# Kernel tuning notes

Measured on AMD Instinct MI355X. Metric: run time of the kernel, lower is better.

## Reference

```python
import jax, jax.numpy as jnp
import numpy as np

B, T, D, H = 2, 4096, 768, 12
HD = D // H  # head_dim = 64


def setup_inputs() -> dict:
    key = jax.random.key(0)
    ks = jax.random.split(key, 6)
    s = 0.02
    return {
        "x": jax.random.normal(ks[0], (B, T, D), dtype=jnp.float32),
        "Wq": jax.random.normal(ks[1], (D, D), dtype=jnp.float32) * s,
        "Wk": jax.random.normal(ks[2], (D, D), dtype=jnp.float32) * s,
        "Wv": jax.random.normal(ks[3], (D, D), dtype=jnp.float32) * s,
        "Wo": jax.random.normal(ks[4], (D, D), dtype=jnp.float32) * s,
        "bo": jnp.zeros((D,), dtype=jnp.float32),
    }


def reference(x, Wq, Wk, Wv, Wo, bo):
    b, t, d = x.shape
    # QKV projections (no bias), reshape to [B, H, T, HD]
    def heads(w):
        return (x @ w.T).reshape(b, t, H, HD).transpose(0, 2, 1, 3)
    q, k, v = heads(Wq), heads(Wk), heads(Wv)
    scores = jnp.einsum("bhqd,bhkd->bhqk", q, k)  # [B,H,T,T]
    causal = jnp.tril(jnp.ones((t, t), dtype=bool))
    scores = jnp.where(causal, scores, -jnp.inf)
    attn = jax.nn.softmax(scores / jnp.sqrt(jnp.float32(HD)), axis=-1)
    ctx = jnp.einsum("bhqk,bhkd->bhqd", attn, v)  # [B,H,T,HD]
    ctx = ctx.transpose(0, 2, 1, 3).reshape(b, t, d)
    return ctx @ Wo.T + bo
```

## Files before the change

kernel.cpp:

```cpp
#include <hip/hip_runtime.h>
#include <hip/hip_bf16.h>
#include <cstdint>
#include <cstddef>

#define B_  2
#define T_  4096
#define D_  768
#define H_  12
#define HD_ 64
#define M_  (B_*T_)

#define SCL 0.18033688f

typedef __bf16 bf16x8 __attribute__((ext_vector_type(8)));
typedef float  f32x4  __attribute__((ext_vector_type(4)));
using bf16 = __hip_bfloat16;

__device__ inline float fexp2(float x) {
  float r; asm("v_exp_f32 %0, %1" : "=v"(r) : "v"(x)); return r;
}
__device__ inline uint32_t fu(float x) { union { float f; uint32_t u; } c; c.f = x; return c.u; }
__device__ inline uint32_t pktr(float a, float b) {
  return __builtin_amdgcn_perm(fu(b), fu(a), 0x07060302);
}
#define GLD16(g, l) __builtin_amdgcn_global_load_lds( \
    (const __attribute__((address_space(1))) uint32_t*)(const void*)(g), \
    (__attribute__((address_space(3))) uint32_t*)(void*)(l), 16, 0, 0)

__global__ void cvt_all(const float* __restrict__ x,
                        const float* __restrict__ w0, const float* __restrict__ w1,
                        const float* __restrict__ w2, const float* __restrict__ w3,
                        bf16* __restrict__ xd,
                        bf16* __restrict__ d0, bf16* __restrict__ d1,
                        bf16* __restrict__ d2, bf16* __restrict__ d3) {
  int blk = blockIdx.x;
  const float* s; bf16* d; int i;
  if (blk < 6144) {
    s = x; d = xd; i = blk * 256 + threadIdx.x;
  } else {
    int q = blk - 6144, which = q / 576, rb = q % 576;
    switch (which) {
      case 0: s = w0; d = d0; break;
      case 1: s = w1; d = d1; break;
      case 2: s = w2; d = d2; break;
      default: s = w3; d = d3; break;
    }
    i = rb * 256 + threadIdx.x;
  }
  float4 v = ((const float4*)s)[i];
  union { bf16 o[4]; uint2 u; } pk;
  pk.o[0] = __float2bfloat16(v.x); pk.o[1] = __float2bfloat16(v.y);
  pk.o[2] = __float2bfloat16(v.z); pk.o[3] = __float2bfloat16(v.w);
  *(uint2*)(d + 4 * (size_t)i) = pk.u;
}

__global__ __launch_bounds__(256) void gemm_qkv(const bf16* __restrict__ x,
                                                const bf16* __restrict__ W0,
                                                const bf16* __restrict__ W1,
                                                const bf16* __restrict__ W2,
                                                bf16* __restrict__ O0,
                                                bf16* __restrict__ O1,
                                                bf16* __restrict__ O2t) {
  __shared__ bf16 As[2][4096];
  __shared__ bf16 Bs[2][4096];
  const int flat = blockIdx.x;
  const int by = flat / 18;
  const int rr = flat % 18;
  const int z  = rr / 6;
  const int bx = rr % 6;
  const bf16* Wz = (z == 0) ? W0 : ((z == 1) ? W1 : W2);
  const char* Ap; const char* Bp; int a0, b0;
  if (z == 2) { Ap = (const char*)x;  a0 = by * 128; Bp = (const char*)Wz; b0 = bx * 128; }
  else        { Ap = (const char*)Wz; a0 = bx * 128; Bp = (const char*)x;  b0 = by * 128; }
  const int t = threadIdx.x;
  const int w = t >> 6, lane = t & 63;
  const int wa = (w >> 1) * 64, wb = (w & 1) * 64;
  const int mi = lane & 15, qd = lane >> 4;

  int aoff[2], boff[2];
  #pragma unroll
  for (int i = 0; i < 2; ++i) {
    int L = i * 256 + t;
    int row = L >> 2, sl = L & 3, c = sl ^ (row & 3);
    aoff[i] = (a0 + row) * 1536 + c * 16;
    boff[i] = (b0 + row) * 1536 + c * 16;
  }
  const int fsw = (qd ^ (mi & 3)) * 8;

  f32x4 acc[4][4] = {};

  #pragma unroll
  for (int i = 0; i < 2; ++i) {
    GLD16(Ap + aoff[i], &As[0][i * 2048 + w * 512]);
    GLD16(Bp + boff[i], &Bs[0][i * 2048 + w * 512]);
  }

  for (int kk = 0; kk < 24; ++kk) {
    __syncthreads();
    const int par = kk & 1;
    if (kk + 1 < 24) {
      const int np = par ^ 1, kb = (kk + 1) * 64;
      #pragma unroll
      for (int i = 0; i < 2; ++i) {
        GLD16(Ap + aoff[i] + kb, &As[np][i * 2048 + w * 512]);
        GLD16(Bp + boff[i] + kb, &Bs[np][i * 2048 + w * 512]);
      }
    }
    bf16x8 af[4], bfr[4];
    #pragma unroll
    for (int at = 0; at < 4; ++at)
      af[at] = *(const bf16x8*)&As[par][(wa + at * 16 + mi) * 32 + fsw];
    #pragma unroll
    for (int bt = 0; bt < 4; ++bt)
      bfr[bt] = *(const bf16x8*)&Bs[par][(wb + bt * 16 + mi) * 32 + fsw];
    #pragma unroll
    for (int at = 0; at < 4; ++at)
      #pragma unroll
      for (int bt = 0; bt < 4; ++bt)
        acc[at][bt] = __builtin_amdgcn_mfma_f32_16x16x32_bf16(af[at], bfr[bt], acc[at][bt], 0, 0, 0);
  }

  if (z == 2) {
    #pragma unroll
    for (int at = 0; at < 4; ++at)
      #pragma unroll
      for (int bt = 0; bt < 4; ++bt) {
        int gr = a0 + wa + at * 16 + qd * 4;
        int gc = b0 + wb + bt * 16 + mi;
        union { bf16 o[4]; uint2 u; } pk;
        #pragma unroll
        for (int r = 0; r < 4; ++r) pk.o[r] = __float2bfloat16(acc[at][bt][r]);
        int bb = gr >> 12, tt = gr & 4095;
        *(uint2*)(O2t + (size_t)bb * 768 * 4096 + (size_t)gc * 4096 + tt) = pk.u;
      }
  } else {
    const float scl = (z == 1) ? SCL : 1.0f;
    bf16* Ob = (z == 0) ? O0 : O1;
    #pragma unroll
    for (int at = 0; at < 4; ++at)
      #pragma unroll
      for (int bt = 0; bt < 4; ++bt) {
        int f0  = a0 + wa + at * 16 + qd * 4;
        int tkn = b0 + wb + bt * 16 + mi;
        union { bf16 o[4]; uint2 u; } pk;
        #pragma unroll
        for (int r = 0; r < 4; ++r) pk.o[r] = __float2bfloat16(acc[at][bt][r] * scl);
        *(uint2*)(Ob + (size_t)tkn * 768 + f0) = pk.u;
      }
  }
}

__global__ __launch_bounds__(256) void gemm_out(const bf16* __restrict__ ctx,
                                                const bf16* __restrict__ Wo,
                                                float* __restrict__ Cf,
                                                const float* __restrict__ bias) {
  __shared__ bf16 As[2][4096];
  __shared__ bf16 Bs[2][4096];
  const int flat = blockIdx.x;
  const int by = flat / 6, bx = flat % 6;
  const char* Ap = (const char*)Wo;  const int a0 = bx * 128;
  const char* Bp = (const char*)ctx; const int b0 = by * 128;
  const int t = threadIdx.x;
  const int w = t >> 6, lane = t & 63;
  const int wa = (w >> 1) * 64, wb = (w & 1) * 64;
  const int mi = lane & 15, qd = lane >> 4;

  int aoff[2], boff[2];
  #pragma unroll
  for (int i = 0; i < 2; ++i) {
    int L = i * 256 + t;
    int row = L >> 2, sl = L & 3, c = sl ^ (row & 3);
    aoff[i] = (a0 + row) * 1536 + c * 16;
    boff[i] = (b0 + row) * 1536 + c * 16;
  }
  const int fsw = (qd ^ (mi & 3)) * 8;

  f32x4 acc[4][4] = {};

  #pragma unroll
  for (int i = 0; i < 2; ++i) {
    GLD16(Ap + aoff[i], &As[0][i * 2048 + w * 512]);
    GLD16(Bp + boff[i], &Bs[0][i * 2048 + w * 512]);
  }

  for (int kk = 0; kk < 24; ++kk) {
    __syncthreads();
    const int par = kk & 1;
    if (kk + 1 < 24) {
      const int np = par ^ 1, kb = (kk + 1) * 64;
      #pragma unroll
      for (int i = 0; i < 2; ++i) {
        GLD16(Ap + aoff[i] + kb, &As[np][i * 2048 + w * 512]);
        GLD16(Bp + boff[i] + kb, &Bs[np][i * 2048 + w * 512]);
      }
    }
    bf16x8 af[4], bfr[4];
    #pragma unroll
    for (int at = 0; at < 4; ++at)
      af[at] = *(const bf16x8*)&As[par][(wa + at * 16 + mi) * 32 + fsw];
    #pragma unroll
    for (int bt = 0; bt < 4; ++bt)
      bfr[bt] = *(const bf16x8*)&Bs[par][(wb + bt * 16 + mi) * 32 + fsw];
    #pragma unroll
    for (int at = 0; at < 4; ++at)
      #pragma unroll
      for (int bt = 0; bt < 4; ++bt)
        acc[at][bt] = __builtin_amdgcn_mfma_f32_16x16x32_bf16(af[at], bfr[bt], acc[at][bt], 0, 0, 0);
  }

  #pragma unroll
  for (int at = 0; at < 4; ++at)
    #pragma unroll
    for (int bt = 0; bt < 4; ++bt) {
      int f0  = a0 + wa + at * 16 + qd * 4;
      int tkn = b0 + wb + bt * 16 + mi;
      float4 bv = *(const float4*)&bias[f0];
      float4 o;
      o.x = acc[at][bt][0] + bv.x; o.y = acc[at][bt][1] + bv.y;
      o.z = acc[at][bt][2] + bv.z; o.w = acc[at][bt][3] + bv.w;
      *(float4*)&Cf[(size_t)tkn * 768 + f0] = o;
    }
}

__global__ __launch_bounds__(256, 4) void flash_attn(const bf16* __restrict__ Q,
                                                     const bf16* __restrict__ K,
                                                     const bf16* __restrict__ Vt,
                                                     bf16* __restrict__ ctx) {
  __shared__ bf16 Ks[2][4096];
  __shared__ bf16 Vs[2][4096];
  __shared__ bf16 Pt[4][1024];
  const int t = threadIdx.x;
  const int w = t >> 6, lane = t & 63;
  const int mi = lane & 15, qd = lane >> 4;
  const int bh   = blockIdx.x % 24;
  const int qrev = blockIdx.x / 24;
  const int q0 = T_ - 64 - qrev * 64;
  const int b = bh / H_, h = bh % H_;
  const size_t bTD = (size_t)b * T_ * D_;
  const char* Kp = (const char*)(K  + bTD + (size_t)h * HD_);
  const char* Vp = (const char*)(Vt + (size_t)b * D_ * T_ + (size_t)h * HD_ * T_);
  const int qw = q0 + w * 16;

  int vkoff[2], vvoff[2];
  #pragma unroll
  for (int i = 0; i < 2; ++i) {
    int L = i * 256 + t;
    int rl = L >> 3, c = (L & 7) ^ (rl & 7);
    vkoff[i] = rl * 1536 + c * 16;
    vvoff[i] = rl * 8192 + c * 16;
  }

  int fidx[4][2];
  #pragma unroll
  for (int jt = 0; jt < 4; ++jt)
    #pragma unroll
    for (int kt = 0; kt < 2; ++kt)
      fidx[jt][kt] = (jt * 16 + mi) * 64 + (((kt * 4 + qd) ^ (mi & 7)) * 8);

  int pwoff[4], proff[2];
  #pragma unroll
  for (int jt = 0; jt < 4; ++jt)
    pwoff[jt] = mi * 64 + ((2 * jt + (qd >> 1)) ^ (mi & 7)) * 8 + (qd & 1) * 4;
  #pragma unroll
  for (int kt = 0; kt < 2; ++kt)
    proff[kt] = mi * 64 + ((4 * kt + qd) ^ (mi & 7)) * 8;

  bf16x8 qf[2];
  const bf16* Qp = Q + bTD + (size_t)h * HD_;
  #pragma unroll
  for (int kt = 0; kt < 2; ++kt)
    qf[kt] = *(const bf16x8*)(Qp + (size_t)(qw + mi) * D_ + kt * 32 + qd * 8);

  f32x4 oacc[4] = {};
  float lst = 0.f;
  const int ntiles = q0 / 64 + 1;

  #pragma unroll
  for (int i = 0; i < 2; ++i) {
    GLD16(Kp + vkoff[i], &Ks[0][i * 2048 + w * 512]);
    GLD16(Vp + vvoff[i], &Vs[0][i * 2048 + w * 512]);
  }

  for (int tt = 0; tt < ntiles; ++tt) {
    __syncthreads();
    const int par = tt & 1;
    if (tt + 1 < ntiles) {
      const size_t j1 = (size_t)(tt + 1) * 64;
      const int np = par ^ 1;
      #pragma unroll
      for (int i = 0; i < 2; ++i) {
        GLD16(Kp + vkoff[i] + j1 * 1536, &Ks[np][i * 2048 + w * 512]);
        GLD16(Vp + vvoff[i] + j1 * 2,    &Vs[np][i * 2048 + w * 512]);
      }
    }
    const int j0 = tt * 64;

    f32x4 sacc[4] = {};
    #pragma unroll
    for (int jt = 0; jt < 4; ++jt)
      #pragma unroll
      for (int kt = 0; kt < 2; ++kt) {
        bf16x8 kf = *(const bf16x8*)&Ks[par][fidx[jt][kt]];
        sacc[jt] = __builtin_amdgcn_mfma_f32_16x16x32_bf16(kf, qf[kt], sacc[jt], 0, 0, 0);
      }

    if (j0 + 63 > qw) {
      const int qg = qw + mi;
      #pragma unroll
      for (int jt = 0; jt < 4; ++jt)
        #pragma unroll
        for (int r = 0; r < 4; ++r) {
          int jg = j0 + jt * 16 + qd * 4 + r;
          if (jg > qg) sacc[jt][r] = -1e30f;
        }
    }

    #pragma unroll
    for (int jt = 0; jt < 4; ++jt) {
      float p0 = fexp2(sacc[jt][0]);
      float p1 = fexp2(sacc[jt][1]);
      float p2 = fexp2(sacc[jt][2]);
      float p3 = fexp2(sacc[jt][3]);
      lst += (p0 + p1) + (p2 + p3);
      union { uint32_t u[2]; uint64_t d; } pw;
      pw.u[0] = pktr(p0, p1);
      pw.u[1] = pktr(p2, p3);
      *(uint64_t*)&Pt[w][pwoff[jt]] = pw.d;
    }

    asm volatile("s_waitcnt lgkmcnt(0)" ::: "memory");

    #pragma unroll
    for (int ktp = 0; ktp < 2; ++ktp) {
      bf16x8 pfx = *(const bf16x8*)&Pt[w][proff[ktp]];
      #pragma unroll
      for (int dt = 0; dt < 4; ++dt) {
        bf16x8 vf = *(const bf16x8*)&Vs[par][fidx[dt][ktp]];
        oacc[dt] = __builtin_amdgcn_mfma_f32_16x16x32_bf16(vf, pfx, oacc[dt], 0, 0, 0);
      }
    }
  }

  float l = lst;
  l += __shfl_xor(l, 16);
  l += __shfl_xor(l, 32);
  float inv = __builtin_amdgcn_rcpf(l);
  const int qg = qw + mi;
  bf16* cp = ctx + bTD + (size_t)qg * D_ + h * HD_ + qd * 4;
  #pragma unroll
  for (int dt = 0; dt < 4; ++dt) {
    union { bf16 o[4]; uint2 u; } pko;
    #pragma unroll
    for (int r = 0; r < 4; ++r) pko.o[r] = __float2bfloat16(oacc[dt][r] * inv);
    *(uint2*)(cp + dt * 16) = pko.u;
  }
}

extern "C" void kernel_launch(void* const* d_in, const int* in_sizes, int n_in,
                              void* d_out, int out_size, void* d_ws, size_t ws_size,
                              hipStream_t stream) {
  const float* x  = (const float*)d_in[0];
  const float* Wq = (const float*)d_in[1];
  const float* Wk = (const float*)d_in[2];
  const float* Wv = (const float*)d_in[3];
  const float* Wo = (const float*)d_in[4];
  const float* bo = (const float*)d_in[5];
  float* out = (float*)d_out;

  char* ws = (char*)d_ws;
  const size_t SZ  = (size_t)M_ * D_ * 2;
  const size_t WSZ = (size_t)D_ * D_ * 2;
  bf16* xb   = (bf16*)(ws);
  bf16* Qb   = (bf16*)(ws + 1 * SZ);
  bf16* Kb   = (bf16*)(ws + 2 * SZ);
  bf16* Vtg  = (bf16*)(ws + 3 * SZ);
  bf16* ctxb = (bf16*)(ws + 4 * SZ);
  bf16* Wqb  = (bf16*)(ws + 5 * SZ);
  bf16* Wkb  = (bf16*)(ws + 5 * SZ + 1 * WSZ);
  bf16* Wvb  = (bf16*)(ws + 5 * SZ + 2 * WSZ);
  bf16* Wob  = (bf16*)(ws + 5 * SZ + 3 * WSZ);

  cvt_all<<<6144 + 4 * 576, 256, 0, stream>>>(x, Wq, Wk, Wv, Wo, xb, Wqb, Wkb, Wvb, Wob);

  gemm_qkv<<<1152, 256, 0, stream>>>(xb, Wqb, Wkb, Wvb, Qb, Kb, Vtg);

  flash_attn<<<(T_ / 64) * B_ * H_, 256, 0, stream>>>(Qb, Kb, Vtg, ctxb);

  gemm_out<<<384, 256, 0, stream>>>(ctxb, Wob, out, bo);
}
```

Before: 244.0 us.

## Keep attention probabilities in registers via permuted K rows; retile output GEMM

```diff
diff --git a/kernel.cpp b/kernel.cpp
--- a/kernel.cpp
+++ b/kernel.cpp
@@ -154,62 +154,61 @@
                                                 const bf16* __restrict__ Wo,
                                                 float* __restrict__ Cf,
                                                 const float* __restrict__ bias) {
-  __shared__ bf16 As[2][4096];
+  __shared__ bf16 As[2][2048];
   __shared__ bf16 Bs[2][4096];
   const int flat = blockIdx.x;
-  const int by = flat / 6, bx = flat % 6;
-  const char* Ap = (const char*)Wo;  const int a0 = bx * 128;
+  const int by = flat / 12, bx = flat % 12;
+  const char* Ap = (const char*)Wo;  const int a0 = bx * 64;
   const char* Bp = (const char*)ctx; const int b0 = by * 128;
   const int t = threadIdx.x;
   const int w = t >> 6, lane = t & 63;
-  const int wa = (w >> 1) * 64, wb = (w & 1) * 64;
+  const int wa = (w >> 1) * 32, wb = (w & 1) * 64;
   const int mi = lane & 15, qd = lane >> 4;
 
-  int aoff[2], boff[2];
+  int aoff, boff[2];
+  { int row = t >> 2, sl = t & 3, c = sl ^ (row & 3);
+    aoff = (a0 + row) * 1536 + c * 16; }
   #pragma unroll
   for (int i = 0; i < 2; ++i) {
     int L = i * 256 + t;
     int row = L >> 2, sl = L & 3, c = sl ^ (row & 3);
-    aoff[i] = (a0 + row) * 1536 + c * 16;
     boff[i] = (b0 + row) * 1536 + c * 16;
   }
   const int fsw = (qd ^ (mi & 3)) * 8;
 
-  f32x4 acc[4][4] = {};
-
-  #pragma unroll
-  for (int i = 0; i < 2; ++i) {
-    GLD16(Ap + aoff[i], &As[0][i * 2048 + w * 512]);
+  f32x4 acc[2][4] = {};
+
+  GLD16(Ap + aoff, &As[0][w * 512]);
+  #pragma unroll
+  for (int i = 0; i < 2; ++i)
     GLD16(Bp + boff[i], &Bs[0][i * 2048 + w * 512]);
-  }
 
   for (int kk = 0; kk < 24; ++kk) {
     __syncthreads();
     const int par = kk & 1;
     if (kk + 1 < 24) {
       const int np = par ^ 1, kb = (kk + 1) * 64;
-      #pragma unroll
-      for (int i = 0; i < 2; ++i) {
-        GLD16(Ap + aoff[i] + kb, &As[np][i * 2048 + w * 512]);
+      GLD16(Ap + aoff + kb, &As[np][w * 512]);
+      #pragma unroll
+      for (int i = 0; i < 2; ++i)
         GLD16(Bp + boff[i] + kb, &Bs[np][i * 2048 + w * 512]);
-      }
-    }
-    bf16x8 af[4], bfr[4];
-    #pragma unroll
-    for (int at = 0; at < 4; ++at)
+    }
+    bf16x8 af[2], bfr[4];
+    #pragma unroll
+    for (int at = 0; at < 2; ++at)
       af[at] = *(const bf16x8*)&As[par][(wa + at * 16 + mi) * 32 + fsw];
     #pragma unroll
     for (int bt = 0; bt < 4; ++bt)
       bfr[bt] = *(const bf16x8*)&Bs[par][(wb + bt * 16 + mi) * 32 + fsw];
     #pragma unroll
-    for (int at = 0; at < 4; ++at)
+    for (int at = 0; at < 2; ++at)
       #pragma unroll
       for (int bt = 0; bt < 4; ++bt)
         acc[at][bt] = __builtin_amdgcn_mfma_f32_16x16x32_bf16(af[at], bfr[bt], acc[at][bt], 0, 0, 0);
   }
 
   #pragma unroll
-  for (int at = 0; at < 4; ++at)
+  for (int at = 0; at < 2; ++at)
     #pragma unroll
     for (int bt = 0; bt < 4; ++bt) {
       int f0  = a0 + wa + at * 16 + qd * 4;
@@ -222,13 +221,12 @@
     }
 }
 
-__global__ __launch_bounds__(256, 4) void flash_attn(const bf16* __restrict__ Q,
+__global__ __launch_bounds__(256, 5) void flash_attn(const bf16* __restrict__ Q,
                                                      const bf16* __restrict__ K,
                                                      const bf16* __restrict__ Vt,
                                                      bf16* __restrict__ ctx) {
   __shared__ bf16 Ks[2][4096];
   __shared__ bf16 Vs[2][4096];
-  __shared__ bf16 Pt[4][1024];
   const int t = threadIdx.x;
   const int w = t >> 6, lane = t & 63;
   const int mi = lane & 15, qd = lane >> 4;
@@ -246,7 +244,8 @@
   for (int i = 0; i < 2; ++i) {
     int L = i * 256 + t;
     int rl = L >> 3, c = (L & 7) ^ (rl & 7);
-    vkoff[i] = rl * 1536 + c * 16;
+    int jrow = (rl & 32) | ((rl & 0xC) << 1) | ((rl & 16) >> 2) | (rl & 3);
+    vkoff[i] = jrow * 1536 + c * 16;
     vvoff[i] = rl * 8192 + c * 16;
   }
 
@@ -256,14 +255,6 @@
     #pragma unroll
     for (int kt = 0; kt < 2; ++kt)
       fidx[jt][kt] = (jt * 16 + mi) * 64 + (((kt * 4 + qd) ^ (mi & 7)) * 8);
-
-  int pwoff[4], proff[2];
-  #pragma unroll
-  for (int jt = 0; jt < 4; ++jt)
-    pwoff[jt] = mi * 64 + ((2 * jt + (qd >> 1)) ^ (mi & 7)) * 8 + (qd & 1) * 4;
-  #pragma unroll
-  for (int kt = 0; kt < 2; ++kt)
-    proff[kt] = mi * 64 + ((4 * kt + qd) ^ (mi & 7)) * 8;
 
   bf16x8 qf[2];
   const bf16* Qp = Q + bTD + (size_t)h * HD_;
@@ -294,8 +285,10 @@
       }
     }
     const int j0 = tt * 64;
+    if (j0 > qw + 15) continue;
 
     f32x4 sacc[4] = {};
+    __builtin_amdgcn_s_setprio(1);
     #pragma unroll
     for (int jt = 0; jt < 4; ++jt)
       #pragma unroll
@@ -303,6 +296,7 @@
         bf16x8 kf = *(const bf16x8*)&Ks[par][fidx[jt][kt]];
         sacc[jt] = __builtin_amdgcn_mfma_f32_16x16x32_bf16(kf, qf[kt], sacc[jt], 0, 0, 0);
       }
+    __builtin_amdgcn_s_setprio(0);
 
     if (j0 + 63 > qw) {
       const int qg = qw + mi;
@@ -310,11 +304,12 @@
       for (int jt = 0; jt < 4; ++jt)
         #pragma unroll
         for (int r = 0; r < 4; ++r) {
-          int jg = j0 + jt * 16 + qd * 4 + r;
+          int jg = j0 + ((jt >> 1) << 5) + (qd << 3) + ((jt & 1) << 2) + r;
           if (jg > qg) sacc[jt][r] = -1e30f;
         }
     }
 
+    uint32_t pu[4][2];
     #pragma unroll
     for (int jt = 0; jt < 4; ++jt) {
       float p0 = fexp2(sacc[jt][0]);
@@ -322,23 +317,27 @@
       float p2 = fexp2(sacc[jt][2]);
       float p3 = fexp2(sacc[jt][3]);
       lst += (p0 + p1) + (p2 + p3);
-      union { uint32_t u[2]; uint64_t d; } pw;
-      pw.u[0] = pktr(p0, p1);
-      pw.u[1] = pktr(p2, p3);
-      *(uint64_t*)&Pt[w][pwoff[jt]] = pw.d;
-    }
-
-    asm volatile("s_waitcnt lgkmcnt(0)" ::: "memory");
-
-    #pragma unroll
-    for (int ktp = 0; ktp < 2; ++ktp) {
-      bf16x8 pfx = *(const bf16x8*)&Pt[w][proff[ktp]];
+      pu[jt][0] = pktr(p0, p1);
+      pu[jt][1] = pktr(p2, p3);
+    }
+    bf16x8 pB[2];
+    #pragma unroll
+    for (int kt = 0; kt < 2; ++kt) {
+      union { uint32_t u[4]; bf16x8 v; } m;
+      m.u[0] = pu[2 * kt][0];     m.u[1] = pu[2 * kt][1];
+      m.u[2] = pu[2 * kt + 1][0]; m.u[3] = pu[2 * kt + 1][1];
+      pB[kt] = m.v;
+    }
+
+    __builtin_amdgcn_s_setprio(1);
+    #pragma unroll
+    for (int kt = 0; kt < 2; ++kt)
       #pragma unroll
       for (int dt = 0; dt < 4; ++dt) {
-        bf16x8 vf = *(const bf16x8*)&Vs[par][fidx[dt][ktp]];
-        oacc[dt] = __builtin_amdgcn_mfma_f32_16x16x32_bf16(vf, pfx, oacc[dt], 0, 0, 0);
-      }
-    }
+        bf16x8 vf = *(const bf16x8*)&Vs[par][fidx[dt][kt]];
+        oacc[dt] = __builtin_amdgcn_mfma_f32_16x16x32_bf16(vf, pB[kt], oacc[dt], 0, 0, 0);
+      }
+    __builtin_amdgcn_s_setprio(0);
   }
 
   float l = lst;
@@ -386,5 +385,5 @@
 
   flash_attn<<<(T_ / 64) * B_ * H_, 256, 0, stream>>>(Qb, Kb, Vtg, ctxb);
 
-  gemm_out<<<384, 256, 0, stream>>>(ctxb, Wob, out, bo);
-}
+  gemm_out<<<768, 256, 0, stream>>>(ctxb, Wob, out, bo);
+}
```

After: 234.1 us. 4.0% less time.
